# Kernel optimization log

Hardware: AMD Instinct MI355X
Metric: run time of the kernel (lower is better)

Reference implementation:

```python
import jax, jax.numpy as jnp
import numpy as np

SAMPLING = 16   # VGG16 feature stride
POOL = 7        # adaptive max pool output size
KMAX = 5        # max bin window; valid for ROI feature extents <= 28 cells
NEG = jnp.float32(-1e30)


def _bin_bounds(s0, L, i):
    # torch AdaptiveMaxPool2d bin i over a length-L crop starting at s0:
    # [s0 + floor(i*L/P), s0 + ceil((i+1)*L/P))
    bs = s0 + (i * L) // POOL
    be = s0 + ((i + 1) * L + POOL - 1) // POOL
    return bs, be


def setup_inputs() -> dict:
    key = jax.random.key(0)
    ks = jax.random.split(key, 12)
    N, C, Hf, Wf = 1024, 512, 50, 84
    Himg, Wimg = Hf * SAMPLING, Wf * SAMPLING
    # post-ReLU VGG features -> non-negative
    featmap = jax.random.uniform(ks[0], (1, C, Hf, Wf), dtype=jnp.float32)
    # ROI boxes [x0, y0, x1, y1] in pixel coords, extents in [32, 448] px
    x0 = jax.random.randint(ks[1], (N,), 0, Wimg - 448)
    y0 = jax.random.randint(ks[2], (N,), 0, Himg - 448)
    w = jax.random.randint(ks[3], (N,), 32, 449)
    h = jax.random.randint(ks[4], (N,), 32, 449)
    roi = jnp.stack([x0, y0, x0 + w, y0 + h], axis=1).astype(jnp.int32)
    d = C * POOL * POOL  # 25088
    W1 = jax.random.normal(ks[5], (d, 4096), dtype=jnp.float32) * 0.01
    b1 = jnp.zeros((4096,), jnp.float32)
    W2 = jax.random.normal(ks[6], (4096, 4096), dtype=jnp.float32) * 0.01
    b2 = jnp.zeros((4096,), jnp.float32)
    Wc = jax.random.normal(ks[7], (4096, 3), dtype=jnp.float32) * 0.01
    bc = jnp.zeros((3,), jnp.float32)
    Wr = jax.random.normal(ks[8], (4096, 12), dtype=jnp.float32) * 0.01
    br = jnp.zeros((12,), jnp.float32)
    return {"featmap": featmap, "roi": roi, "W1": W1, "b1": b1, "W2": W2,
            "b2": b2, "Wc": Wc, "bc": bc, "Wr": Wr, "br": br}


def _roipool(featmap, roi):
    fm = featmap[0]                       # (C, Hf, Wf)
    C, Hf, Wf = fm.shape
    rf = roi // SAMPLING                  # floor, coords are non-negative
    x0, y0, x1, y1 = rf[:, 0], rf[:, 1], rf[:, 2], rf[:, 3]
    # width expand: if x1-x0 <= 1 -> grow right if in-bounds else grow left
    nw = (x1 - x0) <= 1
    x0n = jnp.where(nw & ~(x1 < Wf), x0 - 1, x0)
    x1n = jnp.where(nw & (x1 < Wf), x1 + 1, x1)
    nh = (y1 - y0) <= 1
    y0n = jnp.where(nh & ~(y1 < Hf), y0 - 1, y0)
    y1n = jnp.where(nh & (y1 < Hf), y1 + 1, y1)
    # python slice semantics clamp to array bounds
    xs, xe = jnp.clip(x0n, 0, Wf), jnp.clip(x1n, 0, Wf)
    ys, ye = jnp.clip(y0n, 0, Hf), jnp.clip(y1n, 0, Hf)
    Lx, Ly = xe - xs, ye - ys
    ar = jnp.arange(KMAX)
    rows = []
    for i in range(POOL):                 # fixed 7x7 bins
        hs, he = _bin_bounds(ys, Ly, i)
        h_idx = hs[:, None] + ar          # (N, K)
        h_ok = h_idx < he[:, None]
        h_idx = jnp.clip(h_idx, 0, Hf - 1)
        cols = []
        for j in range(POOL):
            ws_, we_ = _bin_bounds(xs, Lx, j)
            w_idx = ws_[:, None] + ar     # (N, K)
            w_ok = w_idx < we_[:, None]
            w_idx = jnp.clip(w_idx, 0, Wf - 1)
            patch = fm[:, h_idx[:, :, None], w_idx[:, None, :]]  # (C, N, K, K)
            m = h_ok[:, :, None] & w_ok[:, None, :]              # (N, K, K)
            patch = jnp.where(m[None], patch, NEG)
            cols.append(patch.max(axis=(2, 3)))                  # (C, N)
        rows.append(jnp.stack(cols, 0))   # (7, C, N)
    pool = jnp.stack(rows, 0)             # (7, 7, C, N)
    return pool.transpose(3, 2, 0, 1).reshape(roi.shape[0], -1)  # (N, C*49)


def reference(featmap, roi, W1, b1, W2, b2, Wc, bc, Wr, br):
    pooled = _roipool(featmap, roi)       # (N, 25088)
    h = (pooled @ W1 + b1) @ W2 + b2      # two Linears, no activation (as in source)
    output_cls = jax.nn.softmax(h @ Wc + bc, axis=1)
    output_reg = h @ Wr + br
    return output_cls, output_reg
```

## Files before the change

kernel.cpp:

```cpp
#include <hip/hip_runtime.h>
#include <hip/hip_bf16.h>
#include <cstdint>
#include <cstddef>

typedef __attribute__((ext_vector_type(4))) float f32x4;
typedef __attribute__((ext_vector_type(8))) short s16x8;
typedef __attribute__((ext_vector_type(4))) unsigned short u16x4;

__device__ __forceinline__ unsigned short f2bf(float f) {
    union { float f; unsigned u; } v; v.f = f;
    unsigned u = v.u;
    u += 0x7fffu + ((u >> 16) & 1u);
    return (unsigned short)(u >> 16);
}
__device__ __forceinline__ float lo_f(unsigned v) {
    union { unsigned u; float f; } w; w.u = v << 16; return w.f;
}
__device__ __forceinline__ float hi_f(unsigned v) {
    union { unsigned u; float f; } w; w.u = v & 0xffff0000u; return w.f;
}


__global__ __launch_bounds__(256) void prep_wcat(
        const float* __restrict__ Wc, const float* __restrict__ Wr,
        unsigned short* __restrict__ WcatT) {
    int idx = blockIdx.x * 256 + threadIdx.x;
    int i = idx >> 4, j = idx & 15;
    float v = (j < 3) ? Wc[i * 3 + j] : (j < 15) ? Wr[i * 12 + (j - 3)] : 0.f;
    WcatT[(size_t)j * 4096 + i] = f2bf(v);
}

template<bool NT>
__device__ __forceinline__ void skinny_body(
        const float* __restrict__ A, const unsigned short* __restrict__ BT,
        float* __restrict__ partial, int R, int kchunk,
        int bx, int ky, int t) {
    const int lane = t & 63, wave = t >> 6;
    const int r0 = bx * 128 + wave * 16;
    const int k0 = ky * kchunk;
    const int lr = lane & 15, lks = lane >> 4;
    const int steps = kchunk >> 5;
    const float* ap = A + (size_t)(r0 + lr) * 4096 + k0 + lks * 8;
    const unsigned short* bp = BT + (size_t)lr * 4096 + k0 + lks * 8;
    f32x4 acc = {0.f, 0.f, 0.f, 0.f};
    for (int s = 0; s < steps; ++s) {
        f32x4 f0, f1;
        if (NT) {
            f0 = __builtin_nontemporal_load((const f32x4*)(ap + s * 32));
            f1 = __builtin_nontemporal_load((const f32x4*)(ap + s * 32 + 4));
        } else {
            f0 = *(const f32x4*)(ap + s * 32);
            f1 = *(const f32x4*)(ap + s * 32 + 4);
        }
        s16x8 b = *(const s16x8*)(bp + s * 32);
        union { unsigned short us[8]; s16x8 v; } a;
        a.us[0] = f2bf(f0.x); a.us[1] = f2bf(f0.y);
        a.us[2] = f2bf(f0.z); a.us[3] = f2bf(f0.w);
        a.us[4] = f2bf(f1.x); a.us[5] = f2bf(f1.y);
        a.us[6] = f2bf(f1.z); a.us[7] = f2bf(f1.w);
        acc = __builtin_amdgcn_mfma_f32_16x16x32_bf16(a.v, b, acc, 0, 0, 0);
    }
    const int row = r0 + (lane >> 4) * 4;
    float* op = partial + ((size_t)ky * R + row) * 16 + lr;
    #pragma unroll
    for (int q = 0; q < 4; ++q) {
        if (NT) __builtin_nontemporal_store(acc[q], op + q * 16);
        else    op[q * 16] = acc[q];
    }
}

__global__ __launch_bounds__(512) void prepA(
        const float* __restrict__ fm, unsigned short* __restrict__ fmT,
        const float* __restrict__ W2, const unsigned short* __restrict__ WcatT,
        float* __restrict__ partial1) {
    const int g5 = blockIdx.x / 5, r5 = blockIdx.x % 5;
    const int t = threadIdx.x;
    if (r5 < 4) {
        const int unit = g5 * 4 + r5;
        if (unit >= 1056) return;
        __shared__ float tile[2][32][33];
        const int sub = t >> 8, tt = t & 255;
        const int tid = unit * 2 + sub;
        const int p0 = (tid % 132) * 32, c0 = (tid / 132) * 32;
        const int tx = tt & 31, ty = tt >> 5;
        #pragma unroll
        for (int yy = ty; yy < 32; yy += 8) {
            int p = p0 + tx;
            if (p < 4200) tile[sub][yy][tx] = fm[(size_t)(c0 + yy) * 4200 + p];
        }
        __syncthreads();
        #pragma unroll
        for (int yy = ty; yy < 32; yy += 8) {
            int p = p0 + yy;
            if (p < 4200) fmT[(size_t)p * 512 + c0 + tx] = f2bf(tile[sub][tx][yy]);
        }
    } else {
        const int v = g5;
        if (v >= 256) return;
        skinny_body<false>(W2, WcatT, partial1, 4096, 512, v & 31, v >> 5, t);
    }
}

__global__ __launch_bounds__(256) void reduce_wf(
        const float* __restrict__ partial1, const float* __restrict__ b2,
        const float* __restrict__ Wc, const float* __restrict__ Wr,
        const float* __restrict__ bc, const float* __restrict__ br,
        float* __restrict__ Wf16, unsigned short* __restrict__ WfT,
        float* __restrict__ bfv) {
    const int t = threadIdx.x;
    if (blockIdx.x < 256) {
        int idx = blockIdx.x * 256 + t;
        float s = 0.f;
        #pragma unroll
        for (int sp = 0; sp < 8; ++sp) s += partial1[sp * 65536 + idx];
        Wf16[idx] = s;
        int i = idx >> 4, j = idx & 15;
        WfT[(size_t)j * 4096 + i] = f2bf(s);
    } else {
        float acc[15];
        #pragma unroll
        for (int j = 0; j < 15; ++j) acc[j] = 0.f;
        for (int i = t; i < 4096; i += 256) {
            float bv = b2[i];
            #pragma unroll
            for (int j = 0; j < 15; ++j)
                acc[j] += bv * ((j < 3) ? Wc[i * 3 + j] : Wr[i * 12 + (j - 3)]);
        }
        const int lane = t & 63, wv = t >> 6;
        __shared__ float red[4][15];
        #pragma unroll
        for (int j = 0; j < 15; ++j) {
            float x = acc[j];
            #pragma unroll
            for (int off = 32; off >= 1; off >>= 1) x += __shfl_xor(x, off, 64);
            if (lane == 0) red[wv][j] = x;
        }
        __syncthreads();
        if (t < 15)
            bfv[t] = red[0][t] + red[1][t] + red[2][t] + red[3][t]
                   + ((t < 3) ? bc[t] : br[t - 3]);
    }
}

#define PB(NH, NW) { \
    uint2 v[NH * NW]; \
    _Pragma("unroll") for (int r = 0; r < NH; ++r) \
        _Pragma("unroll") for (int s = 0; s < NW; ++s) \
            v[r * NW + s] = *(const uint2*)(base + ho[r] + wo[s]); \
    float a0 = lo_f(v[0].x), a1 = hi_f(v[0].x); \
    float a2 = lo_f(v[0].y), a3 = hi_f(v[0].y); \
    _Pragma("unroll") for (int q = 1; q < NH * NW; ++q) { \
        a0 = fmaxf(a0, lo_f(v[q].x)); a1 = fmaxf(a1, hi_f(v[q].x)); \
        a2 = fmaxf(a2, lo_f(v[q].y)); a3 = fmaxf(a3, hi_f(v[q].y)); } \
    m0 = a0; m1 = a1; m2 = a2; m3 = a3; } break;

__global__ __launch_bounds__(512) void megaB(
        const unsigned short* __restrict__ fmT, const int* __restrict__ roi,
        unsigned short* __restrict__ pooled,
        const float* __restrict__ W1, const unsigned short* __restrict__ WfT,
        float* __restrict__ partial2) {
    const int g5 = blockIdx.x / 5, r5 = blockIdx.x % 5;
    const int t = threadIdx.x;
    if (r5 < 3) {
        const int sb = g5 * 3 + r5;
        if (sb >= 1568) return;
        const int ky = sb / 196, bx = sb % 196;
        skinny_body<true>(W1, WfT, partial2, 25088, 512, bx, ky, t);
    } else {
        const int n = g5 * 2 + (r5 - 3);
        if (n >= 1024) return;
        __shared__ int hoff[7][5], woff[7][5], hcnt[7], wcnt[7];
        if (t == 0) {
            int x0 = roi[n*4+0] / 16, y0 = roi[n*4+1] / 16;
            int x1 = roi[n*4+2] / 16, y1 = roi[n*4+3] / 16;
            if (x1 - x0 <= 1) { if (x1 < 84) x1 += 1; else x0 -= 1; }
            if (y1 - y0 <= 1) { if (y1 < 50) y1 += 1; else y0 -= 1; }
            int xs = min(max(x0, 0), 84), xe = min(max(x1, 0), 84);
            int ys = min(max(y0, 0), 50), ye = min(max(y1, 0), 50);
            int Lx = xe - xs, Ly = ye - ys;
            #pragma unroll
            for (int i = 0; i < 7; ++i) {
                int b0 = ys + (i * Ly) / 7, b1 = ys + ((i + 1) * Ly + 6) / 7;
                hcnt[i] = min(b1, b0 + 5) - b0;
                int c0 = xs + (i * Lx) / 7, c1 = xs + ((i + 1) * Lx + 6) / 7;
                wcnt[i] = min(c1, c0 + 5) - c0;
                #pragma unroll
                for (int q = 0; q < 5; ++q) {
                    hoff[i][q] = (b0 + q) * 43008;
                    woff[i][q] = (c0 + q) * 512;
                }
            }
        }
        __syncthreads();
        const int g = t >> 7;
        const int c4 = (t & 127) * 4;
        const unsigned short* base = fmT + c4;
        unsigned short* orow = pooled + (size_t)n * 25088;
        for (int bp = 0; bp < 13; ++bp) {
            int bin = bp * 4 + g;
            if (bin < 49) {
                int bi = bin / 7, bj = bin - bi * 7;
                int ho[5], wo[5];
                #pragma unroll
                for (int q = 0; q < 5; ++q) { ho[q] = hoff[bi][q]; wo[q] = woff[bj][q]; }
                int nh = hcnt[bi], nw = wcnt[bj];
                float m0, m1, m2, m3;
                switch ((nh - 1) * 5 + (nw - 1)) {
                    case  0: PB(1,1)  case  1: PB(1,2)  case  2: PB(1,3)
                    case  3: PB(1,4)  case  4: PB(1,5)
                    case  5: PB(2,1)  case  6: PB(2,2)  case  7: PB(2,3)
                    case  8: PB(2,4)  case  9: PB(2,5)
                    case 10: PB(3,1)  case 11: PB(3,2)  case 12: PB(3,3)
                    case 13: PB(3,4)  case 14: PB(3,5)
                    case 15: PB(4,1)  case 16: PB(4,2)  case 17: PB(4,3)
                    case 18: PB(4,4)  case 19: PB(4,5)
                    case 20: PB(5,1)  case 21: PB(5,2)  case 22: PB(5,3)
                    case 23: PB(5,4)  case 24: PB(5,5)
                    default: m0 = m1 = m2 = m3 = 0.f; break;
                }
                u16x4 o;
                o.x = f2bf(m0); o.y = f2bf(m1); o.z = f2bf(m2); o.w = f2bf(m3);
                __builtin_nontemporal_store(o, (u16x4*)(orow + bin * 512 + c4));
            }
        }
    }
}

__global__ __launch_bounds__(256) void reduce_wbig(
        const float* __restrict__ partial2, const float* __restrict__ Wf16,
        const float* __restrict__ bfv, const float* __restrict__ b1,
        unsigned short* __restrict__ WbigT, float* __restrict__ bbig) {
    const int t = threadIdx.x;
    if (blockIdx.x < 98) {
        const int r = blockIdx.x * 256 + t;
        float sj[16];
        #pragma unroll
        for (int j = 0; j < 16; ++j) sj[j] = 0.f;
        #pragma unroll
        for (int sp = 0; sp < 8; ++sp) {
            const float4* pp = (const float4*)(partial2 + ((size_t)sp * 25088 + r) * 16);
            float4 a = pp[0], b = pp[1], c = pp[2], d = pp[3];
            sj[0] += a.x; sj[1] += a.y; sj[2]  += a.z; sj[3]  += a.w;
            sj[4] += b.x; sj[5] += b.y; sj[6]  += b.z; sj[7]  += b.w;
            sj[8] += c.x; sj[9] += c.y; sj[10] += c.z; sj[11] += c.w;
            sj[12] += d.x; sj[13] += d.y; sj[14] += d.z; sj[15] += d.w;
        }
        const int c = r / 49, bin = r - c * 49;
        const int p = bin * 512 + c;
        #pragma unroll
        for (int j = 0; j < 16; ++j)
            WbigT[(size_t)j * 25088 + p] = f2bf(sj[j]);
    } else {
        float acc[15];
        #pragma unroll
        for (int j = 0; j < 15; ++j) acc[j] = 0.f;
        for (int i = t; i < 4096; i += 256) {
            float bv = b1[i];
            #pragma unroll
            for (int j = 0; j < 15; ++j) acc[j] += bv * Wf16[i * 16 + j];
        }
        const int lane = t & 63, wv = t >> 6;
        __shared__ float red[4][15];
        #pragma unroll
        for (int j = 0; j < 15; ++j) {
            float x = acc[j];
            #pragma unroll
            for (int off = 32; off >= 1; off >>= 1) x += __shfl_xor(x, off, 64);
            if (lane == 0) red[wv][j] = x;
        }
        __syncthreads();
        if (t < 16) {
            float s = 0.f;
            if (t < 15)
                s = red[0][t] + red[1][t] + red[2][t] + red[3][t] + bfv[t];
            bbig[t] = s;
        }
    }
}

__global__ __launch_bounds__(256) void final_gemm(
        const unsigned short* __restrict__ pooled,
        const unsigned short* __restrict__ WbigT,
        float* __restrict__ partialG) {
    const int t = threadIdx.x, lane = t & 63, wave = t >> 6;
    const int m0 = blockIdx.x * 16, kz = blockIdx.y;
    const int lr = lane & 15, lks = lane >> 4;
    f32x4 acc = {0.f, 0.f, 0.f, 0.f};
    const unsigned short* arow = pooled + (size_t)(m0 + lr) * 25088 + kz * 3136 + lks * 8;
    const unsigned short* brow = WbigT + (size_t)lr * 25088 + kz * 3136 + lks * 8;
    for (int s = wave; s < 98; s += 4) {
        s16x8 a = __builtin_nontemporal_load((const s16x8*)(arow + s * 32));
        s16x8 b = *(const s16x8*)(brow + s * 32);
        acc = __builtin_amdgcn_mfma_f32_16x16x32_bf16(a, b, acc, 0, 0, 0);
    }
    __shared__ float red[4][64][4];
    #pragma unroll
    for (int r = 0; r < 4; ++r) red[wave][lane][r] = acc[r];
    __syncthreads();
    if (wave == 0) {
        #pragma unroll
        for (int r = 0; r < 4; ++r) {
            float s = red[0][lane][r] + red[1][lane][r] + red[2][lane][r] + red[3][lane][r];
            int row = m0 + (lane >> 4) * 4 + r;
            partialG[((size_t)kz * 1024 + row) * 16 + (lane & 15)] = s;
        }
    }
}

__global__ __launch_bounds__(256) void finalize_kernel(
        const float* __restrict__ partialG, const float* __restrict__ bbig,
        float* __restrict__ out) {
    const int m = blockIdx.x * 256 + threadIdx.x;
    float v[15];
    #pragma unroll
    for (int j = 0; j < 15; ++j) v[j] = bbig[j];
    for (int kz = 0; kz < 8; ++kz) {
        const float* p = partialG + ((size_t)kz * 1024 + m) * 16;
        #pragma unroll
        for (int j = 0; j < 15; ++j) v[j] += p[j];
    }
    float mx = fmaxf(v[0], fmaxf(v[1], v[2]));
    float e0 = expf(v[0] - mx), e1 = expf(v[1] - mx), e2 = expf(v[2] - mx);
    float inv = 1.f / (e0 + e1 + e2);
    out[m * 3 + 0] = e0 * inv;
    out[m * 3 + 1] = e1 * inv;
    out[m * 3 + 2] = e2 * inv;
    #pragma unroll
    for (int j = 3; j < 15; ++j) out[3072 + m * 12 + (j - 3)] = v[j];
}

extern "C" void kernel_launch(void* const* d_in, const int* in_sizes, int n_in,
                              void* d_out, int out_size, void* d_ws, size_t ws_size,
                              hipStream_t stream) {
    const float* featmap = (const float*)d_in[0];
    const int*   roi     = (const int*)d_in[1];
    const float* W1      = (const float*)d_in[2];
    const float* b1      = (const float*)d_in[3];
    const float* W2      = (const float*)d_in[4];
    const float* b2      = (const float*)d_in[5];
    const float* Wc      = (const float*)d_in[6];
    const float* bc      = (const float*)d_in[7];
    const float* Wr      = (const float*)d_in[8];
    const float* br      = (const float*)d_in[9];
    float* out = (float*)d_out;

    char* ws = (char*)d_ws;
    unsigned short* pooled   = (unsigned short*)(ws);
    unsigned short* fmT      = (unsigned short*)(ws + 51380224);
    unsigned short* WcatT    = (unsigned short*)(ws + 55681024);
    unsigned short* WfT      = (unsigned short*)(ws + 55812096);
    float*          Wf16     = (float*)        (ws + 55943168);
    float*          bfv      = (float*)        (ws + 56205312);
    float*          bbig     = (float*)        (ws + 56205376);
    float*          partial1 = (float*)        (ws + 56205440);
    float*          partial2 = (float*)        (ws + 60399744);
    unsigned short* WbigT    = (unsigned short*)(ws + 111779968);
    float*          partialG = (float*)        (ws + 112582784);

    prep_wcat<<<256, 256, 0, stream>>>(Wc, Wr, WcatT);
    prepA<<<1320, 512, 0, stream>>>(featmap, fmT, W2, WcatT, partial1);
    reduce_wf<<<257, 256, 0, stream>>>(partial1, b2, Wc, Wr, bc, br, Wf16, WfT, bfv);
    megaB<<<2615, 512, 0, stream>>>(fmT, roi, pooled, W1, WfT, partial2);
    reduce_wbig<<<99, 256, 0, stream>>>(partial2, Wf16, bfv, b1, WbigT, bbig);
    final_gemm<<<dim3(64, 8), 256, 0, stream>>>(pooled, WbigT, partialG);
    finalize_kernel<<<4, 256, 0, stream>>>(partialG, bbig, out);
}
```

Before: 214.4 us.

## Fuse all stages into one persistent cooperative kernel with grid syncs

Replaces seven separate kernel launches with a single cooperative persistent kernel of 256 blocks. Each stage runs as a strided loop over virtual blocks, with grid.sync between stages; the main W1/pooling stage pulls work through an atomic counter. The Wc/Wr transpose kernel is dropped and the bf16 B operand is now built inline in the W2 GEMM. This targets launch gaps and tail effects, at the cost of reduced parallelism in the small stages and grid-barrier overhead. A fallback multi-kernel path runs if the cooperative launch fails.

```diff
diff --git a/kernel.cpp b/kernel.cpp
--- a/kernel.cpp
+++ b/kernel.cpp
@@ -1,7 +1,10 @@
 #include <hip/hip_runtime.h>
 #include <hip/hip_bf16.h>
+#include <hip/hip_cooperative_groups.h>
 #include <cstdint>
 #include <cstddef>
+
+namespace cg = cooperative_groups;
 
 typedef __attribute__((ext_vector_type(4))) float f32x4;
 typedef __attribute__((ext_vector_type(8))) short s16x8;
@@ -21,124 +24,109 @@
 }
 
 
-__global__ __launch_bounds__(256) void prep_wcat(
-        const float* __restrict__ Wc, const float* __restrict__ Wr,
-        unsigned short* __restrict__ WcatT) {
-    int idx = blockIdx.x * 256 + threadIdx.x;
-    int i = idx >> 4, j = idx & 15;
-    float v = (j < 3) ? Wc[i * 3 + j] : (j < 15) ? Wr[i * 12 + (j - 3)] : 0.f;
-    WcatT[(size_t)j * 4096 + i] = f2bf(v);
-}
-
-template<bool NT>
-__device__ __forceinline__ void skinny_body(
-        const float* __restrict__ A, const unsigned short* __restrict__ BT,
-        float* __restrict__ partial, int R, int kchunk,
-        int bx, int ky, int t) {
-    const int lane = t & 63, wave = t >> 6;
-    const int r0 = bx * 128 + wave * 16;
-    const int k0 = ky * kchunk;
-    const int lr = lane & 15, lks = lane >> 4;
-    const int steps = kchunk >> 5;
-    const float* ap = A + (size_t)(r0 + lr) * 4096 + k0 + lks * 8;
-    const unsigned short* bp = BT + (size_t)lr * 4096 + k0 + lks * 8;
-    f32x4 acc = {0.f, 0.f, 0.f, 0.f};
-    for (int s = 0; s < steps; ++s) {
-        f32x4 f0, f1;
-        if (NT) {
-            f0 = __builtin_nontemporal_load((const f32x4*)(ap + s * 32));
-            f1 = __builtin_nontemporal_load((const f32x4*)(ap + s * 32 + 4));
-        } else {
-            f0 = *(const f32x4*)(ap + s * 32);
-            f1 = *(const f32x4*)(ap + s * 32 + 4);
-        }
-        s16x8 b = *(const s16x8*)(bp + s * 32);
-        union { unsigned short us[8]; s16x8 v; } a;
-        a.us[0] = f2bf(f0.x); a.us[1] = f2bf(f0.y);
-        a.us[2] = f2bf(f0.z); a.us[3] = f2bf(f0.w);
-        a.us[4] = f2bf(f1.x); a.us[5] = f2bf(f1.y);
-        a.us[6] = f2bf(f1.z); a.us[7] = f2bf(f1.w);
-        acc = __builtin_amdgcn_mfma_f32_16x16x32_bf16(a.v, b, acc, 0, 0, 0);
-    }
-    const int row = r0 + (lane >> 4) * 4;
-    float* op = partial + ((size_t)ky * R + row) * 16 + lr;
-    #pragma unroll
-    for (int q = 0; q < 4; ++q) {
-        if (NT) __builtin_nontemporal_store(acc[q], op + q * 16);
-        else    op[q * 16] = acc[q];
-    }
-}
-
-__global__ __launch_bounds__(512) void prepA(
-        const float* __restrict__ fm, unsigned short* __restrict__ fmT,
-        const float* __restrict__ W2, const unsigned short* __restrict__ WcatT,
-        float* __restrict__ partial1) {
-    const int g5 = blockIdx.x / 5, r5 = blockIdx.x % 5;
-    const int t = threadIdx.x;
-    if (r5 < 4) {
-        const int unit = g5 * 4 + r5;
-        if (unit >= 1056) return;
-        __shared__ float tile[2][32][33];
-        const int sub = t >> 8, tt = t & 255;
-        const int tid = unit * 2 + sub;
-        const int p0 = (tid % 132) * 32, c0 = (tid / 132) * 32;
-        const int tx = tt & 31, ty = tt >> 5;
-        #pragma unroll
-        for (int yy = ty; yy < 32; yy += 8) {
-            int p = p0 + tx;
-            if (p < 4200) tile[sub][yy][tx] = fm[(size_t)(c0 + yy) * 4200 + p];
-        }
-        __syncthreads();
-        #pragma unroll
-        for (int yy = ty; yy < 32; yy += 8) {
-            int p = p0 + yy;
-            if (p < 4200) fmT[(size_t)p * 512 + c0 + tx] = f2bf(tile[sub][tx][yy]);
-        }
+struct MP {
+    const float* fm; const int* roi;
+    const float* W1; const float* b1; const float* W2; const float* b2;
+    const float* Wc; const float* bc; const float* Wr; const float* br;
+    float* out;
+    unsigned short* pooled; unsigned short* fmT; unsigned short* WfT;
+    float* Wf16; float* bfv; float* bbig;
+    float* partial1; float* partial2;
+    unsigned short* WbigT; float* partialG;
+    unsigned* counter;
+};
+
+__device__ void p0_unit(const MP& p, int vb, int t) {
+    if (vb < 1056) {
+        __shared__ float tile[32][65];
+        const int p0 = (vb % 66) * 64, c0 = (vb / 66) * 32;
+        {
+            const int pp = t & 63, cc = t >> 6;
+            #pragma unroll
+            for (int k = 0; k < 4; ++k) {
+                int c = c0 + cc + 8 * k;
+                if (p0 + pp < 4200) tile[cc + 8 * k][pp] = p.fm[(size_t)c * 4200 + p0 + pp];
+            }
+        }
+        __syncthreads();
+        {
+            const int c = t & 31, pr = t >> 5;
+            #pragma unroll
+            for (int k = 0; k < 4; ++k) {
+                int pp = p0 + pr + 16 * k;
+                if (pp < 4200) p.fmT[(size_t)pp * 512 + c0 + c] = f2bf(tile[c][pr + 16 * k]);
+            }
+        }
+        __syncthreads();
     } else {
-        const int v = g5;
-        if (v >= 256) return;
-        skinny_body<false>(W2, WcatT, partial1, 4096, 512, v & 31, v >> 5, t);
-    }
-}
-
-__global__ __launch_bounds__(256) void reduce_wf(
-        const float* __restrict__ partial1, const float* __restrict__ b2,
-        const float* __restrict__ Wc, const float* __restrict__ Wr,
-        const float* __restrict__ bc, const float* __restrict__ br,
-        float* __restrict__ Wf16, unsigned short* __restrict__ WfT,
-        float* __restrict__ bfv) {
-    const int t = threadIdx.x;
-    if (blockIdx.x < 256) {
-        int idx = blockIdx.x * 256 + t;
+        const int v = vb - 1056;
+        const int bx = v & 31, ky = v >> 5;
+        const int lane = t & 63, wave = t >> 6;
+        const int r0 = bx * 128 + wave * 16;
+        const int k0 = ky * 512;
+        const int lr = lane & 15, lks = lane >> 4;
+        const float* ap = p.W2 + (size_t)(r0 + lr) * 4096 + k0 + lks * 8;
+        f32x4 acc = {0.f, 0.f, 0.f, 0.f};
+        for (int s = 0; s < 16; ++s) {
+            f32x4 f0 = *(const f32x4*)(ap + s * 32);
+            f32x4 f1 = *(const f32x4*)(ap + s * 32 + 4);
+            union { unsigned short us[8]; s16x8 v; } a, b;
+            const int i0 = k0 + s * 32 + lks * 8;
+            #pragma unroll
+            for (int e = 0; e < 8; ++e) {
+                int i = i0 + e;
+                float bv = (lr < 3) ? p.Wc[i * 3 + lr] : (lr < 15) ? p.Wr[i * 12 + lr - 3] : 0.f;
+                b.us[e] = f2bf(bv);
+            }
+            a.us[0] = f2bf(f0.x); a.us[1] = f2bf(f0.y);
+            a.us[2] = f2bf(f0.z); a.us[3] = f2bf(f0.w);
+            a.us[4] = f2bf(f1.x); a.us[5] = f2bf(f1.y);
+            a.us[6] = f2bf(f1.z); a.us[7] = f2bf(f1.w);
+            acc = __builtin_amdgcn_mfma_f32_16x16x32_bf16(a.v, b.v, acc, 0, 0, 0);
+        }
+        const int row = r0 + (lane >> 4) * 4;
+        float* op = p.partial1 + ((size_t)ky * 4096 + row) * 16 + lr;
+        #pragma unroll
+        for (int q = 0; q < 4; ++q) op[q * 16] = acc[q];
+    }
+}
+
+__device__ void p1_unit(const MP& p, int vb, int t) {
+    const int lane = t & 63, wv = t >> 6;
+    if (vb < 128) {
+        int idx = vb * 512 + t;
         float s = 0.f;
         #pragma unroll
-        for (int sp = 0; sp < 8; ++sp) s += partial1[sp * 65536 + idx];
-        Wf16[idx] = s;
+        for (int sp = 0; sp < 8; ++sp) s += p.partial1[sp * 65536 + idx];
+        p.Wf16[idx] = s;
         int i = idx >> 4, j = idx & 15;
-        WfT[(size_t)j * 4096 + i] = f2bf(s);
+        p.WfT[(size_t)j * 4096 + i] = f2bf(s);
     } else {
+        __shared__ float red15[8][15];
         float acc[15];
         #pragma unroll
         for (int j = 0; j < 15; ++j) acc[j] = 0.f;
-        for (int i = t; i < 4096; i += 256) {
-            float bv = b2[i];
+        for (int i = t; i < 4096; i += 512) {
+            float bv = p.b2[i];
             #pragma unroll
             for (int j = 0; j < 15; ++j)
-                acc[j] += bv * ((j < 3) ? Wc[i * 3 + j] : Wr[i * 12 + (j - 3)]);
-        }
-        const int lane = t & 63, wv = t >> 6;
-        __shared__ float red[4][15];
+                acc[j] += bv * ((j < 3) ? p.Wc[i * 3 + j] : p.Wr[i * 12 + (j - 3)]);
+        }
         #pragma unroll
         for (int j = 0; j < 15; ++j) {
             float x = acc[j];
             #pragma unroll
             for (int off = 32; off >= 1; off >>= 1) x += __shfl_xor(x, off, 64);
-            if (lane == 0) red[wv][j] = x;
-        }
-        __syncthreads();
-        if (t < 15)
-            bfv[t] = red[0][t] + red[1][t] + red[2][t] + red[3][t]
-                   + ((t < 3) ? bc[t] : br[t - 3]);
+            if (lane == 0) red15[wv][j] = x;
+        }
+        __syncthreads();
+        if (t < 15) {
+            float s = 0.f;
+            #pragma unroll
+            for (int w = 0; w < 8; ++w) s += red15[w][t];
+            p.bfv[t] = s + ((t < 3) ? p.bc[t] : p.br[t - 3]);
+        }
+        __syncthreads();
     }
 }
 
@@ -154,25 +142,42 @@
         a2 = fmaxf(a2, lo_f(v[q].y)); a3 = fmaxf(a3, hi_f(v[q].y)); } \
     m0 = a0; m1 = a1; m2 = a2; m3 = a3; } break;
 
-__global__ __launch_bounds__(512) void megaB(
-        const unsigned short* __restrict__ fmT, const int* __restrict__ roi,
-        unsigned short* __restrict__ pooled,
-        const float* __restrict__ W1, const unsigned short* __restrict__ WfT,
-        float* __restrict__ partial2) {
-    const int g5 = blockIdx.x / 5, r5 = blockIdx.x % 5;
-    const int t = threadIdx.x;
+__device__ void p2_unit(const MP& p, int vb, int t) {
+    const int g5 = vb / 5, r5 = vb % 5;
     if (r5 < 3) {
         const int sb = g5 * 3 + r5;
         if (sb >= 1568) return;
-        const int ky = sb / 196, bx = sb % 196;
-        skinny_body<true>(W1, WfT, partial2, 25088, 512, bx, ky, t);
+        const int bx = sb % 196, ky = sb / 196;
+        const int lane = t & 63, wave = t >> 6;
+        const int r0 = bx * 128 + wave * 16;
+        const int k0 = ky * 512;
+        const int lr = lane & 15, lks = lane >> 4;
+        const float* ap = p.W1 + (size_t)(r0 + lr) * 4096 + k0 + lks * 8;
+        const unsigned short* bp = p.WfT + (size_t)lr * 4096 + k0 + lks * 8;
+        f32x4 acc = {0.f, 0.f, 0.f, 0.f};
+        #pragma unroll 4
+        for (int s = 0; s < 16; ++s) {
+            f32x4 f0 = __builtin_nontemporal_load((const f32x4*)(ap + s * 32));
+            f32x4 f1 = __builtin_nontemporal_load((const f32x4*)(ap + s * 32 + 4));
+            s16x8 b = *(const s16x8*)(bp + s * 32);
+            union { unsigned short us[8]; s16x8 v; } a;
+            a.us[0] = f2bf(f0.x); a.us[1] = f2bf(f0.y);
+            a.us[2] = f2bf(f0.z); a.us[3] = f2bf(f0.w);
+            a.us[4] = f2bf(f1.x); a.us[5] = f2bf(f1.y);
+            a.us[6] = f2bf(f1.z); a.us[7] = f2bf(f1.w);
+            acc = __builtin_amdgcn_mfma_f32_16x16x32_bf16(a.v, b, acc, 0, 0, 0);
+        }
+        const int row = r0 + (lane >> 4) * 4;
+        float* op = p.partial2 + ((size_t)ky * 25088 + row) * 16 + lr;
+        #pragma unroll
+        for (int q = 0; q < 4; ++q) __builtin_nontemporal_store(acc[q], op + q * 16);
     } else {
         const int n = g5 * 2 + (r5 - 3);
         if (n >= 1024) return;
         __shared__ int hoff[7][5], woff[7][5], hcnt[7], wcnt[7];
         if (t == 0) {
-            int x0 = roi[n*4+0] / 16, y0 = roi[n*4+1] / 16;
-            int x1 = roi[n*4+2] / 16, y1 = roi[n*4+3] / 16;
+            int x0 = p.roi[n*4+0] / 16, y0 = p.roi[n*4+1] / 16;
+            int x1 = p.roi[n*4+2] / 16, y1 = p.roi[n*4+3] / 16;
             if (x1 - x0 <= 1) { if (x1 < 84) x1 += 1; else x0 -= 1; }
             if (y1 - y0 <= 1) { if (y1 < 50) y1 += 1; else y0 -= 1; }
             int xs = min(max(x0, 0), 84), xe = min(max(x1, 0), 84);
@@ -194,8 +199,8 @@
         __syncthreads();
         const int g = t >> 7;
         const int c4 = (t & 127) * 4;
-        const unsigned short* base = fmT + c4;
-        unsigned short* orow = pooled + (size_t)n * 25088;
+        const unsigned short* base = p.fmT + c4;
+        unsigned short* orow = p.pooled + (size_t)n * 25088;
         for (int bp = 0; bp < 13; ++bp) {
             int bin = bp * 4 + g;
             if (bin < 49) {
@@ -223,22 +228,20 @@
                 __builtin_nontemporal_store(o, (u16x4*)(orow + bin * 512 + c4));
             }
         }
-    }
-}
-
-__global__ __launch_bounds__(256) void reduce_wbig(
-        const float* __restrict__ partial2, const float* __restrict__ Wf16,
-        const float* __restrict__ bfv, const float* __restrict__ b1,
-        unsigned short* __restrict__ WbigT, float* __restrict__ bbig) {
-    const int t = threadIdx.x;
-    if (blockIdx.x < 98) {
-        const int r = blockIdx.x * 256 + t;
+        __syncthreads();
+    }
+}
+
+__device__ void p3_unit(const MP& p, int vb, int t) {
+    const int lane = t & 63, wv = t >> 6;
+    if (vb < 49) {
+        const int r = vb * 512 + t;
         float sj[16];
         #pragma unroll
         for (int j = 0; j < 16; ++j) sj[j] = 0.f;
         #pragma unroll
         for (int sp = 0; sp < 8; ++sp) {
-            const float4* pp = (const float4*)(partial2 + ((size_t)sp * 25088 + r) * 16);
+            const float4* pp = (const float4*)(p.partial2 + ((size_t)sp * 25088 + r) * 16);
             float4 a = pp[0], b = pp[1], c = pp[2], d = pp[3];
             sj[0] += a.x; sj[1] += a.y; sj[2]  += a.z; sj[3]  += a.w;
             sj[4] += b.x; sj[5] += b.y; sj[6]  += b.z; sj[7]  += b.w;
@@ -246,122 +249,165 @@
             sj[12] += d.x; sj[13] += d.y; sj[14] += d.z; sj[15] += d.w;
         }
         const int c = r / 49, bin = r - c * 49;
-        const int p = bin * 512 + c;
+        const int pk = bin * 512 + c;
         #pragma unroll
         for (int j = 0; j < 16; ++j)
-            WbigT[(size_t)j * 25088 + p] = f2bf(sj[j]);
+            p.WbigT[(size_t)j * 25088 + pk] = f2bf(sj[j]);
     } else {
+        __shared__ float red15b[8][15];
         float acc[15];
         #pragma unroll
         for (int j = 0; j < 15; ++j) acc[j] = 0.f;
-        for (int i = t; i < 4096; i += 256) {
-            float bv = b1[i];
-            #pragma unroll
-            for (int j = 0; j < 15; ++j) acc[j] += bv * Wf16[i * 16 + j];
-        }
-        const int lane = t & 63, wv = t >> 6;
-        __shared__ float red[4][15];
+        for (int i = t; i < 4096; i += 512) {
+            float bv = p.b1[i];
+            #pragma unroll
+            for (int j = 0; j < 15; ++j) acc[j] += bv * p.Wf16[i * 16 + j];
+        }
         #pragma unroll
         for (int j = 0; j < 15; ++j) {
             float x = acc[j];
             #pragma unroll
             for (int off = 32; off >= 1; off >>= 1) x += __shfl_xor(x, off, 64);
-            if (lane == 0) red[wv][j] = x;
+            if (lane == 0) red15b[wv][j] = x;
         }
         __syncthreads();
         if (t < 16) {
             float s = 0.f;
-            if (t < 15)
-                s = red[0][t] + red[1][t] + red[2][t] + red[3][t] + bfv[t];
-            bbig[t] = s;
-        }
-    }
-}
-
-__global__ __launch_bounds__(256) void final_gemm(
-        const unsigned short* __restrict__ pooled,
-        const unsigned short* __restrict__ WbigT,
-        float* __restrict__ partialG) {
-    const int t = threadIdx.x, lane = t & 63, wave = t >> 6;
-    const int m0 = blockIdx.x * 16, kz = blockIdx.y;
+            if (t < 15) {
+                #pragma unroll
+                for (int w = 0; w < 8; ++w) s += red15b[w][t];
+                s += p.bfv[t];
+            }
+            p.bbig[t] = s;
+        }
+        __syncthreads();
+    }
+}
+
+__device__ void p4_unit(const MP& p, int vb, int t) {
+    __shared__ float redG[8][64][4];
+    const int lane = t & 63, wv = t >> 6;
+    const int m0 = (vb & 63) * 16, kz = vb >> 6;
     const int lr = lane & 15, lks = lane >> 4;
     f32x4 acc = {0.f, 0.f, 0.f, 0.f};
-    const unsigned short* arow = pooled + (size_t)(m0 + lr) * 25088 + kz * 3136 + lks * 8;
-    const unsigned short* brow = WbigT + (size_t)lr * 25088 + kz * 3136 + lks * 8;
-    for (int s = wave; s < 98; s += 4) {
+    const unsigned short* arow = p.pooled + (size_t)(m0 + lr) * 25088 + kz * 3136 + lks * 8;
+    const unsigned short* brow = p.WbigT + (size_t)lr * 25088 + kz * 3136 + lks * 8;
+    for (int s = wv; s < 98; s += 8) {
         s16x8 a = __builtin_nontemporal_load((const s16x8*)(arow + s * 32));
         s16x8 b = *(const s16x8*)(brow + s * 32);
         acc = __builtin_amdgcn_mfma_f32_16x16x32_bf16(a, b, acc, 0, 0, 0);
     }
-    __shared__ float red[4][64][4];
     #pragma unroll
-    for (int r = 0; r < 4; ++r) red[wave][lane][r] = acc[r];
+    for (int r = 0; r < 4; ++r) redG[wv][lane][r] = acc[r];
     __syncthreads();
-    if (wave == 0) {
+    if (wv == 0) {
         #pragma unroll
         for (int r = 0; r < 4; ++r) {
-            float s = red[0][lane][r] + red[1][lane][r] + red[2][lane][r] + red[3][lane][r];
+            float s = 0.f;
+            #pragma unroll
+            for (int w = 0; w < 8; ++w) s += redG[w][lane][r];
             int row = m0 + (lane >> 4) * 4 + r;
-            partialG[((size_t)kz * 1024 + row) * 16 + (lane & 15)] = s;
-        }
-    }
-}
-
-__global__ __launch_bounds__(256) void finalize_kernel(
-        const float* __restrict__ partialG, const float* __restrict__ bbig,
-        float* __restrict__ out) {
-    const int m = blockIdx.x * 256 + threadIdx.x;
+            p.partialG[((size_t)kz * 1024 + row) * 16 + (lane & 15)] = s;
+        }
+    }
+    __syncthreads();
+}
+
+__device__ void p5_unit(const MP& p, int vb, int t) {
+    const int m = vb * 512 + t;
     float v[15];
     #pragma unroll
-    for (int j = 0; j < 15; ++j) v[j] = bbig[j];
+    for (int j = 0; j < 15; ++j) v[j] = p.bbig[j];
     for (int kz = 0; kz < 8; ++kz) {
-        const float* p = partialG + ((size_t)kz * 1024 + m) * 16;
-        #pragma unroll
-        for (int j = 0; j < 15; ++j) v[j] += p[j];
+        const float* pp = p.partialG + ((size_t)kz * 1024 + m) * 16;
+        #pragma unroll
+        for (int j = 0; j < 15; ++j) v[j] += pp[j];
     }
     float mx = fmaxf(v[0], fmaxf(v[1], v[2]));
     float e0 = expf(v[0] - mx), e1 = expf(v[1] - mx), e2 = expf(v[2] - mx);
     float inv = 1.f / (e0 + e1 + e2);
-    out[m * 3 + 0] = e0 * inv;
-    out[m * 3 + 1] = e1 * inv;
-    out[m * 3 + 2] = e2 * inv;
+    p.out[m * 3 + 0] = e0 * inv;
+    p.out[m * 3 + 1] = e1 * inv;
+    p.out[m * 3 + 2] = e2 * inv;
     #pragma unroll
-    for (int j = 3; j < 15; ++j) out[3072 + m * 12 + (j - 3)] = v[j];
-}
+    for (int j = 3; j < 15; ++j) p.out[3072 + m * 12 + (j - 3)] = v[j];
+}
+
+__global__ __launch_bounds__(512, 2) void mega(MP p) {
+    cg::grid_group grid = cg::this_grid();
+    const int t = threadIdx.x;
+    const int bid = blockIdx.x, nb = gridDim.x;
+    __shared__ int svb;
+
+    if (bid == 0 && t == 0) *p.counter = 0;
+    for (int vb = bid; vb < 1312; vb += nb) p0_unit(p, vb, t);
+    grid.sync();
+    for (int vb = bid; vb < 129; vb += nb) p1_unit(p, vb, t);
+    grid.sync();
+    while (true) {
+        if (t == 0) svb = (int)atomicAdd(p.counter, 1u);
+        __syncthreads();
+        const int vb = svb;
+        if (vb >= 2615) break;
+        p2_unit(p, vb, t);
+        __syncthreads();
+    }
+    grid.sync();
+    for (int vb = bid; vb < 50; vb += nb) p3_unit(p, vb, t);
+    grid.sync();
+    for (int vb = bid; vb < 512; vb += nb) p4_unit(p, vb, t);
+    grid.sync();
+    for (int vb = bid; vb < 2; vb += nb) p5_unit(p, vb, t);
+}
+
+__global__ __launch_bounds__(512) void fb0(MP p) {
+    if (blockIdx.x == 0 && threadIdx.x == 0) *p.counter = 0;
+    p0_unit(p, blockIdx.x, threadIdx.x);
+}
+__global__ __launch_bounds__(512) void fb1(MP p) { p1_unit(p, blockIdx.x, threadIdx.x); }
+__global__ __launch_bounds__(512) void fb2(MP p) { p2_unit(p, blockIdx.x, threadIdx.x); }
+__global__ __launch_bounds__(512) void fb3(MP p) { p3_unit(p, blockIdx.x, threadIdx.x); }
+__global__ __launch_bounds__(512) void fb4(MP p) { p4_unit(p, blockIdx.x, threadIdx.x); }
+__global__ __launch_bounds__(512) void fb5(MP p) { p5_unit(p, blockIdx.x, threadIdx.x); }
 
 extern "C" void kernel_launch(void* const* d_in, const int* in_sizes, int n_in,
                               void* d_out, int out_size, void* d_ws, size_t ws_size,
                               hipStream_t stream) {
-    const float* featmap = (const float*)d_in[0];
-    const int*   roi     = (const int*)d_in[1];
-    const float* W1      = (const float*)d_in[2];
-    const float* b1      = (const float*)d_in[3];
-    const float* W2      = (const float*)d_in[4];
-    const float* b2      = (const float*)d_in[5];
-    const float* Wc      = (const float*)d_in[6];
-    const float* bc      = (const float*)d_in[7];
-    const float* Wr      = (const float*)d_in[8];
-    const float* br      = (const float*)d_in[9];
-    float* out = (float*)d_out;
-
     char* ws = (char*)d_ws;
-    unsigned short* pooled   = (unsigned short*)(ws);
-    unsigned short* fmT      = (unsigned short*)(ws + 51380224);
-    unsigned short* WcatT    = (unsigned short*)(ws + 55681024);
-    unsigned short* WfT      = (unsigned short*)(ws + 55812096);
-    float*          Wf16     = (float*)        (ws + 55943168);
-    float*          bfv      = (float*)        (ws + 56205312);
-    float*          bbig     = (float*)        (ws + 56205376);
-    float*          partial1 = (float*)        (ws + 56205440);
-    float*          partial2 = (float*)        (ws + 60399744);
-    unsigned short* WbigT    = (unsigned short*)(ws + 111779968);
-    float*          partialG = (float*)        (ws + 112582784);
-
-    prep_wcat<<<256, 256, 0, stream>>>(Wc, Wr, WcatT);
-    prepA<<<1320, 512, 0, stream>>>(featmap, fmT, W2, WcatT, partial1);
-    reduce_wf<<<257, 256, 0, stream>>>(partial1, b2, Wc, Wr, bc, br, Wf16, WfT, bfv);
-    megaB<<<2615, 512, 0, stream>>>(fmT, roi, pooled, W1, WfT, partial2);
-    reduce_wbig<<<99, 256, 0, stream>>>(partial2, Wf16, bfv, b1, WbigT, bbig);
-    final_gemm<<<dim3(64, 8), 256, 0, stream>>>(pooled, WbigT, partialG);
-    finalize_kernel<<<4, 256, 0, stream>>>(partialG, bbig, out);
-}
+    MP p;
+    p.fm   = (const float*)d_in[0];
+    p.roi  = (const int*)d_in[1];
+    p.W1   = (const float*)d_in[2];
+    p.b1   = (const float*)d_in[3];
+    p.W2   = (const float*)d_in[4];
+    p.b2   = (const float*)d_in[5];
+    p.Wc   = (const float*)d_in[6];
+    p.bc   = (const float*)d_in[7];
+    p.Wr   = (const float*)d_in[8];
+    p.br   = (const float*)d_in[9];
+    p.out  = (float*)d_out;
+    p.pooled   = (unsigned short*)(ws);
+    p.fmT      = (unsigned short*)(ws + 51380224);
+    p.WfT      = (unsigned short*)(ws + 55681024);
+    p.Wf16     = (float*)         (ws + 55812096);
+    p.bfv      = (float*)         (ws + 56074240);
+    p.bbig     = (float*)         (ws + 56074304);
+    p.counter  = (unsigned*)      (ws + 56074368);
+    p.partial1 = (float*)         (ws + 56074432);
+    p.partial2 = (float*)         (ws + 60268800);
+    p.WbigT    = (unsigned short*)(ws + 111649024);
+    p.partialG = (float*)         (ws + 112451840);
+
+    void* kargs[] = { &p };
+    hipError_t err = hipLaunchCooperativeKernel((const void*)mega, dim3(256),
+                                                dim3(512), kargs, 0, stream);
+    if (err != hipSuccess) {
+        (void)hipGetLastError();
+        fb0<<<1312, 512, 0, stream>>>(p);
+        fb1<<<129, 512, 0, stream>>>(p);
+        fb2<<<2615, 512, 0, stream>>>(p);
+        fb3<<<50, 512, 0, stream>>>(p);
+        fb4<<<512, 512, 0, stream>>>(p);
+        fb5<<<2, 512, 0, stream>>>(p);
+    }
+}
```

New measurement: 383.5 us. +78.9%, slower.

## Fuse Wc/Wr packing into prepA and shrink megaB blocks to 256 threads

Applied to the files above, without the earlier changes.

Removes the separate prep_wcat kernel: the skinny W2 GEMM blocks in prepA now read Wc/Wr directly and convert them to bf16 on the fly, at the cost of strided scalar loads in the inner loop. megaB is relaunched with 256-thread blocks, so each GEMM block now covers 64 rows instead of 128 and each ROI-pool block handles one ROI with two bin groups. The grid and interleave ratio change to match (3 GEMM blocks per 1 pool block). The aim is to save one launch and improve load balance and occupancy in the main fused kernel.

```diff
diff --git a/kernel.cpp b/kernel.cpp
--- a/kernel.cpp
+++ b/kernel.cpp
@@ -21,58 +21,10 @@
 }
 
 
-__global__ __launch_bounds__(256) void prep_wcat(
-        const float* __restrict__ Wc, const float* __restrict__ Wr,
-        unsigned short* __restrict__ WcatT) {
-    int idx = blockIdx.x * 256 + threadIdx.x;
-    int i = idx >> 4, j = idx & 15;
-    float v = (j < 3) ? Wc[i * 3 + j] : (j < 15) ? Wr[i * 12 + (j - 3)] : 0.f;
-    WcatT[(size_t)j * 4096 + i] = f2bf(v);
-}
-
-template<bool NT>
-__device__ __forceinline__ void skinny_body(
-        const float* __restrict__ A, const unsigned short* __restrict__ BT,
-        float* __restrict__ partial, int R, int kchunk,
-        int bx, int ky, int t) {
-    const int lane = t & 63, wave = t >> 6;
-    const int r0 = bx * 128 + wave * 16;
-    const int k0 = ky * kchunk;
-    const int lr = lane & 15, lks = lane >> 4;
-    const int steps = kchunk >> 5;
-    const float* ap = A + (size_t)(r0 + lr) * 4096 + k0 + lks * 8;
-    const unsigned short* bp = BT + (size_t)lr * 4096 + k0 + lks * 8;
-    f32x4 acc = {0.f, 0.f, 0.f, 0.f};
-    for (int s = 0; s < steps; ++s) {
-        f32x4 f0, f1;
-        if (NT) {
-            f0 = __builtin_nontemporal_load((const f32x4*)(ap + s * 32));
-            f1 = __builtin_nontemporal_load((const f32x4*)(ap + s * 32 + 4));
-        } else {
-            f0 = *(const f32x4*)(ap + s * 32);
-            f1 = *(const f32x4*)(ap + s * 32 + 4);
-        }
-        s16x8 b = *(const s16x8*)(bp + s * 32);
-        union { unsigned short us[8]; s16x8 v; } a;
-        a.us[0] = f2bf(f0.x); a.us[1] = f2bf(f0.y);
-        a.us[2] = f2bf(f0.z); a.us[3] = f2bf(f0.w);
-        a.us[4] = f2bf(f1.x); a.us[5] = f2bf(f1.y);
-        a.us[6] = f2bf(f1.z); a.us[7] = f2bf(f1.w);
-        acc = __builtin_amdgcn_mfma_f32_16x16x32_bf16(a.v, b, acc, 0, 0, 0);
-    }
-    const int row = r0 + (lane >> 4) * 4;
-    float* op = partial + ((size_t)ky * R + row) * 16 + lr;
-    #pragma unroll
-    for (int q = 0; q < 4; ++q) {
-        if (NT) __builtin_nontemporal_store(acc[q], op + q * 16);
-        else    op[q * 16] = acc[q];
-    }
-}
-
 __global__ __launch_bounds__(512) void prepA(
         const float* __restrict__ fm, unsigned short* __restrict__ fmT,
-        const float* __restrict__ W2, const unsigned short* __restrict__ WcatT,
-        float* __restrict__ partial1) {
+        const float* __restrict__ W2, const float* __restrict__ Wc,
+        const float* __restrict__ Wr, float* __restrict__ partial1) {
     const int g5 = blockIdx.x / 5, r5 = blockIdx.x % 5;
     const int t = threadIdx.x;
     if (r5 < 4) {
@@ -97,7 +49,34 @@
     } else {
         const int v = g5;
         if (v >= 256) return;
-        skinny_body<false>(W2, WcatT, partial1, 4096, 512, v & 31, v >> 5, t);
+        const int bx = v & 31, ky = v >> 5;
+        const int lane = t & 63, wave = t >> 6;
+        const int r0 = bx * 128 + wave * 16;
+        const int k0 = ky * 512;
+        const int lr = lane & 15, lks = lane >> 4;
+        const float* ap = W2 + (size_t)(r0 + lr) * 4096 + k0 + lks * 8;
+        f32x4 acc = {0.f, 0.f, 0.f, 0.f};
+        for (int s = 0; s < 16; ++s) {
+            f32x4 f0 = *(const f32x4*)(ap + s * 32);
+            f32x4 f1 = *(const f32x4*)(ap + s * 32 + 4);
+            union { unsigned short us[8]; s16x8 v; } a, b;
+            const int i0 = k0 + s * 32 + lks * 8;
+            #pragma unroll
+            for (int e = 0; e < 8; ++e) {
+                int i = i0 + e;
+                float bv = (lr < 3) ? Wc[i * 3 + lr] : (lr < 15) ? Wr[i * 12 + lr - 3] : 0.f;
+                b.us[e] = f2bf(bv);
+            }
+            a.us[0] = f2bf(f0.x); a.us[1] = f2bf(f0.y);
+            a.us[2] = f2bf(f0.z); a.us[3] = f2bf(f0.w);
+            a.us[4] = f2bf(f1.x); a.us[5] = f2bf(f1.y);
+            a.us[6] = f2bf(f1.z); a.us[7] = f2bf(f1.w);
+            acc = __builtin_amdgcn_mfma_f32_16x16x32_bf16(a.v, b.v, acc, 0, 0, 0);
+        }
+        const int row = r0 + (lane >> 4) * 4;
+        float* op = partial1 + ((size_t)ky * 4096 + row) * 16 + lr;
+        #pragma unroll
+        for (int q = 0; q < 4; ++q) op[q * 16] = acc[q];
     }
 }
 
@@ -154,20 +133,42 @@
         a2 = fmaxf(a2, lo_f(v[q].y)); a3 = fmaxf(a3, hi_f(v[q].y)); } \
     m0 = a0; m1 = a1; m2 = a2; m3 = a3; } break;
 
-__global__ __launch_bounds__(512) void megaB(
+__global__ __launch_bounds__(256) void megaB(
         const unsigned short* __restrict__ fmT, const int* __restrict__ roi,
         unsigned short* __restrict__ pooled,
         const float* __restrict__ W1, const unsigned short* __restrict__ WfT,
         float* __restrict__ partial2) {
-    const int g5 = blockIdx.x / 5, r5 = blockIdx.x % 5;
+    const int g4 = blockIdx.x >> 2, r4 = blockIdx.x & 3;
     const int t = threadIdx.x;
-    if (r5 < 3) {
-        const int sb = g5 * 3 + r5;
-        if (sb >= 1568) return;
-        const int ky = sb / 196, bx = sb % 196;
-        skinny_body<true>(W1, WfT, partial2, 25088, 512, bx, ky, t);
+    if (r4 < 3) {
+        const int sb = g4 * 3 + r4;
+        if (sb >= 3136) return;
+        const int bx = sb % 392, ky = sb / 392;
+        const int lane = t & 63, wave = t >> 6;
+        const int r0 = bx * 64 + wave * 16;
+        const int k0 = ky * 512;
+        const int lr = lane & 15, lks = lane >> 4;
+        const float* ap = W1 + (size_t)(r0 + lr) * 4096 + k0 + lks * 8;
+        const unsigned short* bp = WfT + (size_t)lr * 4096 + k0 + lks * 8;
+        f32x4 acc = {0.f, 0.f, 0.f, 0.f};
+        #pragma unroll 4
+        for (int s = 0; s < 16; ++s) {
+            f32x4 f0 = __builtin_nontemporal_load((const f32x4*)(ap + s * 32));
+            f32x4 f1 = __builtin_nontemporal_load((const f32x4*)(ap + s * 32 + 4));
+            s16x8 b = *(const s16x8*)(bp + s * 32);
+            union { unsigned short us[8]; s16x8 v; } a;
+            a.us[0] = f2bf(f0.x); a.us[1] = f2bf(f0.y);
+            a.us[2] = f2bf(f0.z); a.us[3] = f2bf(f0.w);
+            a.us[4] = f2bf(f1.x); a.us[5] = f2bf(f1.y);
+            a.us[6] = f2bf(f1.z); a.us[7] = f2bf(f1.w);
+            acc = __builtin_amdgcn_mfma_f32_16x16x32_bf16(a.v, b, acc, 0, 0, 0);
+        }
+        const int row = r0 + (lane >> 4) * 4;
+        float* op = partial2 + ((size_t)ky * 25088 + row) * 16 + lr;
+        #pragma unroll
+        for (int q = 0; q < 4; ++q) __builtin_nontemporal_store(acc[q], op + q * 16);
     } else {
-        const int n = g5 * 2 + (r5 - 3);
+        const int n = g4;
         if (n >= 1024) return;
         __shared__ int hoff[7][5], woff[7][5], hcnt[7], wcnt[7];
         if (t == 0) {
@@ -196,8 +197,8 @@
         const int c4 = (t & 127) * 4;
         const unsigned short* base = fmT + c4;
         unsigned short* orow = pooled + (size_t)n * 25088;
-        for (int bp = 0; bp < 13; ++bp) {
-            int bin = bp * 4 + g;
+        for (int bp = 0; bp < 25; ++bp) {
+            int bin = bp * 2 + g;
             if (bin < 49) {
                 int bi = bin / 7, bj = bin - bi * 7;
                 int ho[5], wo[5];
@@ -347,20 +348,18 @@
     char* ws = (char*)d_ws;
     unsigned short* pooled   = (unsigned short*)(ws);
     unsigned short* fmT      = (unsigned short*)(ws + 51380224);
-    unsigned short* WcatT    = (unsigned short*)(ws + 55681024);
-    unsigned short* WfT      = (unsigned short*)(ws + 55812096);
-    float*          Wf16     = (float*)        (ws + 55943168);
-    float*          bfv      = (float*)        (ws + 56205312);
-    float*          bbig     = (float*)        (ws + 56205376);
-    float*          partial1 = (float*)        (ws + 56205440);
-    float*          partial2 = (float*)        (ws + 60399744);
-    unsigned short* WbigT    = (unsigned short*)(ws + 111779968);
-    float*          partialG = (float*)        (ws + 112582784);
-
-    prep_wcat<<<256, 256, 0, stream>>>(Wc, Wr, WcatT);
-    prepA<<<1320, 512, 0, stream>>>(featmap, fmT, W2, WcatT, partial1);
+    unsigned short* WfT      = (unsigned short*)(ws + 55681024);
+    float*          Wf16     = (float*)        (ws + 55812096);
+    float*          bfv      = (float*)        (ws + 56074240);
+    float*          bbig     = (float*)        (ws + 56074304);
+    float*          partial1 = (float*)        (ws + 56074432);
+    float*          partial2 = (float*)        (ws + 60268800);
+    unsigned short* WbigT    = (unsigned short*)(ws + 111649024);
+    float*          partialG = (float*)        (ws + 112451840);
+
+    prepA<<<1320, 512, 0, stream>>>(featmap, fmT, W2, Wc, Wr, partial1);
     reduce_wf<<<257, 256, 0, stream>>>(partial1, b2, Wc, Wr, bc, br, Wf16, WfT, bfv);
-    megaB<<<2615, 512, 0, stream>>>(fmT, roi, pooled, W1, WfT, partial2);
+    megaB<<<4184, 256, 0, stream>>>(fmT, roi, pooled, W1, WfT, partial2);
     reduce_wbig<<<99, 256, 0, stream>>>(partial2, Wf16, bfv, b1, WbigT, bbig);
     final_gemm<<<dim3(64, 8), 256, 0, stream>>>(pooled, WbigT, partialG);
     finalize_kernel<<<4, 256, 0, stream>>>(partialG, bbig, out);
```

Measured after the change: 225.5 us. 5.2% more time.
